# Kernel optimization log

Hardware: AMD Instinct MI355X
Metric: run time of the kernel (lower is better)

Reference implementation:

```python
import jax, jax.numpy as jnp
import numpy as np

EPS = 1e-5

def _patches(x, k, stride, pad):
    # x: [B, C, H, W] -> [B, L, C*k*k] with patch features ordered (c, kh, kw)
    # matching torch unfold / adder2d weight layout [Cout, Cin, kh, kw].
    B, C, H, W = x.shape
    xp = jnp.pad(x, ((0, 0), (0, 0), (pad, pad), (pad, pad)))
    Ho = (H + 2 * pad - k) // stride + 1
    Wo = (W + 2 * pad - k) // stride + 1
    cols = [xp[:, :, i:i + stride * Ho:stride, j:j + stride * Wo:stride]
            for i in range(k) for j in range(k)]
    p = jnp.stack(cols, axis=2)                      # [B, C, k*k, Ho, Wo]
    p = p.reshape(B, C * k * k, Ho * Wo)             # [B, K, L]
    return p.transpose(0, 2, 1), Ho, Wo              # [B, L, K]


def adder2d(x, w, stride, pad):
    # AdderNet layer: out[n,co,h,w] = -sum_{ci,kh,kw} |x_patch - w[co]|
    B = x.shape[0]
    Cout, Cin, k, _ = w.shape
    P, Ho, Wo = _patches(x, k, stride, pad)          # [B, L, K]
    Wf = w.reshape(Cout, Cin * k * k)                # [Cout, K]

    @jax.checkpoint
    def per_out(wrow):                               # wrow: [K]
        return -jnp.sum(jnp.abs(P - wrow), axis=-1)  # [B, L]

    out = jax.lax.map(per_out, Wf)                   # [Cout, B, L]
    return out.transpose(1, 0, 2).reshape(B, Cout, Ho, Wo)


def batchnorm(x, gamma, beta):
    # training-mode BatchNorm2d: batch statistics over (N, H, W)
    mu = jnp.mean(x, axis=(0, 2, 3), keepdims=True)
    var = jnp.var(x, axis=(0, 2, 3), keepdims=True)
    xn = (x - mu) * jax.lax.rsqrt(var + EPS)
    return xn * gamma[None, :, None, None] + beta[None, :, None, None]


def setup_inputs() -> dict:
    key = jax.random.key(0)
    kx, kw1, kw2 = jax.random.split(key, 3)
    B, C, H, W = 32, 64, 32, 32
    return {
        "x": jax.random.normal(kx, (B, C, H, W), dtype=jnp.float32),
        "w1": jax.random.normal(kw1, (C, C, 3, 3), dtype=jnp.float32),
        "g1": jnp.ones((C,), dtype=jnp.float32),
        "b1": jnp.zeros((C,), dtype=jnp.float32),
        "w2": jax.random.normal(kw2, (C, C, 3, 3), dtype=jnp.float32),
        "g2": jnp.ones((C,), dtype=jnp.float32),
        "b2": jnp.zeros((C,), dtype=jnp.float32),
    }


def reference(x, w1, g1, b1, w2, g2, b2):
    out = adder2d(x, w1, stride=1, pad=1)
    out = jax.nn.relu(batchnorm(out, g1, b1))
    out = adder2d(out, w2, stride=1, pad=1)
    out = batchnorm(out, g2, b2)
    return jax.nn.relu(out + x)
```

## Files before the change

kernel.cpp:

```cpp
#include <hip/hip_runtime.h>

#define CH    64
#define HWHW  1024
#define CHW   65536
#define NPIX  32768.0f
#define KDIM  576

#define QSCALE 524288.0f
#define QBIAS  4194304.5f
#define Q0     4194304u
#define QINV   1.9073486328125e-6f

__device__ __forceinline__ unsigned quantf(float x) {
  return (unsigned)fmaf(x, QSCALE, QBIAS);
}

__device__ __forceinline__ unsigned sad_acc(unsigned x, unsigned w, unsigned a) {
  unsigned d;
  asm("v_sad_u32 %0, %1, %2, %3" : "=v"(d) : "v"(x), "s"(w), "v"(a));
  return d;
}

__global__ __launch_bounds__(256) void prep_kernel(
    const float* __restrict__ w1, const float* __restrict__ w2,
    unsigned* __restrict__ wt1, unsigned* __restrict__ wt2,
    float* __restrict__ stats) {
  int i = blockIdx.x * 256 + threadIdx.x;
  if (i < 256) stats[i] = 0.0f;
  if (i < CH * KDIM) {
    int co = i / KDIM, k = i % KDIM;
    wt1[k * CH + co] = quantf(w1[i]);
    wt2[k * CH + co] = quantf(w2[i]);
  }
}

__global__ __launch_bounds__(256, 4) void adder_kernel(
    const float* __restrict__ xin,
    const unsigned* __restrict__ wt,
    float* __restrict__ out,
    float* __restrict__ stats) {
  const int cog  = blockIdx.x;
  const int rg   = blockIdx.y;
  const int n    = blockIdx.z;
  const int tid  = threadIdx.x;
  const int lane = tid & 63;
  const int wv   = __builtin_amdgcn_readfirstlane(tid >> 6);
  const int co0  = cog * 4;
  const int r0   = lane >> 3;
  const int c0   = (lane & 7) * 4;

  __shared__ unsigned xs[2][4][10][37];
  __shared__ unsigned red[64][17];
  const int XSHALF = 4 * 10 * 37;

  const int i0 = tid,       ws0 = i0 / 80, rem0 = i0 % 80;
  const int row0 = rem0 >> 3, c40 = rem0 & 7;
  const int hr0 = rg * 8 - 1 + row0;
  const int i1 = tid + 256, ws1 = i1 / 80, rem1 = i1 % 80;
  const int row1 = rem1 >> 3, c41 = rem1 & 7;
  const int hr1 = rg * 8 - 1 + row1;
  const bool val0 = (hr0 >= 0) && (hr0 < 32);
  const bool val1 = (tid < 64) && (hr1 >= 0) && (hr1 < 32);
  const float* g0 = xin + n * CHW + ws0 * 16 * HWHW + hr0 * 32 + c40 * 4;
  const float* g1 = xin + n * CHW + ws1 * 16 * HWHW + hr1 * 32 + c41 * 4;
  unsigned* l0 = &xs[0][ws0][row0][1 + c40 * 4];
  unsigned* l1 = &xs[0][ws1][row1][1 + c41 * 4];

  float4 a0, a1;
  if (val0) a0 = *(const float4*)g0;
  if (val1) a1 = *(const float4*)g1;
  {
    unsigned* p = (unsigned*)xs;
    for (int i = tid; i < 2 * XSHALF; i += 256) p[i] = Q0;
  }
  __syncthreads();
  if (val0) { l0[0] = quantf(a0.x); l0[1] = quantf(a0.y); l0[2] = quantf(a0.z); l0[3] = quantf(a0.w); }
  if (val1) { l1[0] = quantf(a1.x); l1[1] = quantf(a1.y); l1[2] = quantf(a1.z); l1[3] = quantf(a1.w); }
  __syncthreads();

  const unsigned* wtb = wt + (wv * 144) * 64 + co0;
  unsigned wA[12], wB[12];
  auto LOADW = [&](unsigned* dst, int p) {
    const unsigned* wp = wtb + p * 192;
#pragma unroll
    for (int kw = 0; kw < 3; ++kw)
#pragma unroll
      for (int co = 0; co < 4; ++co) dst[kw * 4 + co] = wp[kw * 64 + co];
  };

  unsigned acc[4][4];
#pragma unroll
  for (int co = 0; co < 4; ++co)
#pragma unroll
    for (int j = 0; j < 4; ++j) acc[co][j] = 0u;

  auto COMPUTE = [&](const unsigned* w, int bufsel, int kh) {
    unsigned xv[6];
#pragma unroll
    for (int j = 0; j < 6; ++j) xv[j] = xs[bufsel][wv][r0 + kh][c0 + j];
#pragma unroll
    for (int kw = 0; kw < 3; ++kw)
#pragma unroll
      for (int co = 0; co < 4; ++co) {
        unsigned ww = w[kw * 4 + co];
        acc[co][0] = sad_acc(xv[kw + 0], ww, acc[co][0]);
        acc[co][1] = sad_acc(xv[kw + 1], ww, acc[co][1]);
        acc[co][2] = sad_acc(xv[kw + 2], ww, acc[co][2]);
        acc[co][3] = sad_acc(xv[kw + 3], ww, acc[co][3]);
      }
  };

  LOADW(wA, 0);
  for (int ci = 0; ci < 16; ci += 2) {
    const int p = ci * 3;
    float4 b0, b1;
    if (val0) b0 = *(const float4*)(g0 + (ci + 1) * HWHW);
    if (val1) b1 = *(const float4*)(g1 + (ci + 1) * HWHW);
    LOADW(wB, p + 1);
    COMPUTE(wA, 0, 0);
    LOADW(wA, p + 2);
    COMPUTE(wB, 0, 1);
    LOADW(wB, p + 3);
    COMPUTE(wA, 0, 2);
    if (val0) { unsigned* d = l0 + XSHALF; d[0] = quantf(b0.x); d[1] = quantf(b0.y); d[2] = quantf(b0.z); d[3] = quantf(b0.w); }
    if (val1) { unsigned* d = l1 + XSHALF; d[0] = quantf(b1.x); d[1] = quantf(b1.y); d[2] = quantf(b1.z); d[3] = quantf(b1.w); }
    __syncthreads();
    const bool more = (ci + 2) < 16;
    float4 e0, e1;
    if (more && val0) e0 = *(const float4*)(g0 + (ci + 2) * HWHW);
    if (more && val1) e1 = *(const float4*)(g1 + (ci + 2) * HWHW);
    LOADW(wA, p + 4);
    COMPUTE(wB, 1, 0);
    LOADW(wB, p + 5);
    COMPUTE(wA, 1, 1);
    { int pn = more ? p + 6 : 0; LOADW(wA, pn); }
    COMPUTE(wB, 1, 2);
    if (more && val0) { l0[0] = quantf(e0.x); l0[1] = quantf(e0.y); l0[2] = quantf(e0.z); l0[3] = quantf(e0.w); }
    if (more && val1) { l1[0] = quantf(e1.x); l1[1] = quantf(e1.y); l1[2] = quantf(e1.z); l1[3] = quantf(e1.w); }
    __syncthreads();
  }

  unsigned* af = &acc[0][0];
  for (int src = 1; src < 4; ++src) {
    if (wv == src) {
#pragma unroll
      for (int j = 0; j < 16; ++j) red[lane][j] = af[j];
    }
    __syncthreads();
    if (wv == 0) {
#pragma unroll
      for (int j = 0; j < 16; ++j) af[j] += red[lane][j];
    }
    __syncthreads();
  }

  if (wv == 0) {
    const int ob = n * CHW + (rg * 8 + r0) * 32 + c0;
#pragma unroll
    for (int co = 0; co < 4; ++co) {
      float t0 = -(float)acc[co][0] * QINV;
      float t1 = -(float)acc[co][1] * QINV;
      float t2 = -(float)acc[co][2] * QINV;
      float t3 = -(float)acc[co][3] * QINV;
      *(float4*)(out + ob + (co0 + co) * HWHW) = make_float4(t0, t1, t2, t3);
      float sm = t0 + t1 + t2 + t3;
      float sq = t0 * t0 + t1 * t1 + t2 * t2 + t3 * t3;
#pragma unroll
      for (int m = 1; m < 64; m <<= 1) {
        sm += __shfl_xor(sm, m);
        sq += __shfl_xor(sq, m);
      }
      if (lane == 0) {
        atomicAdd(stats + co0 + co, sm);
        atomicAdd(stats + 64 + co0 + co, sq);
      }
    }
  }
}

__global__ __launch_bounds__(256) void bnrelu_kernel(
    const float* __restrict__ A, const float* __restrict__ stats,
    const float* __restrict__ g, const float* __restrict__ b,
    float* __restrict__ B) {
  int i = blockIdx.x * 256 + threadIdx.x;
  int c = (i >> 8) & 63;
  float mu  = stats[c] * (1.0f / NPIX);
  float var = fmaf(-mu, mu, stats[64 + c] * (1.0f / NPIX));
  float rs  = rsqrtf(var + 1e-5f);
  float ga  = g[c] * rs;
  float be  = fmaf(-mu, ga, b[c]);
  float4 v = ((const float4*)A)[i];
  v.x = fmaxf(fmaf(v.x, ga, be), 0.0f);
  v.y = fmaxf(fmaf(v.y, ga, be), 0.0f);
  v.z = fmaxf(fmaf(v.z, ga, be), 0.0f);
  v.w = fmaxf(fmaf(v.w, ga, be), 0.0f);
  ((float4*)B)[i] = v;
}

__global__ __launch_bounds__(256) void final_kernel(
    const float* __restrict__ Cbuf, const float* __restrict__ stats,
    const float* __restrict__ g, const float* __restrict__ b,
    const float* __restrict__ xres, float* __restrict__ out) {
  int i = blockIdx.x * 256 + threadIdx.x;
  int c = (i >> 8) & 63;
  float mu  = stats[c] * (1.0f / NPIX);
  float var = fmaf(-mu, mu, stats[64 + c] * (1.0f / NPIX));
  float rs  = rsqrtf(var + 1e-5f);
  float ga  = g[c] * rs;
  float be  = fmaf(-mu, ga, b[c]);
  float4 v = ((const float4*)Cbuf)[i];
  float4 xr = ((const float4*)xres)[i];
  v.x = fmaxf(fmaf(v.x, ga, be) + xr.x, 0.0f);
  v.y = fmaxf(fmaf(v.y, ga, be) + xr.y, 0.0f);
  v.z = fmaxf(fmaf(v.z, ga, be) + xr.z, 0.0f);
  v.w = fmaxf(fmaf(v.w, ga, be) + xr.w, 0.0f);
  ((float4*)out)[i] = v;
}

extern "C" void kernel_launch(void* const* d_in, const int* in_sizes, int n_in,
                              void* d_out, int out_size, void* d_ws, size_t ws_size,
                              hipStream_t stream) {
  const float* x  = (const float*)d_in[0];
  const float* w1 = (const float*)d_in[1];
  const float* g1 = (const float*)d_in[2];
  const float* b1 = (const float*)d_in[3];
  const float* w2 = (const float*)d_in[4];
  const float* g2 = (const float*)d_in[5];
  const float* b2 = (const float*)d_in[6];
  float* outp = (float*)d_out;

  float* ws = (float*)d_ws;
  const size_t NEL = 2097152;
  float*    bufA  = ws;
  float*    bufB  = ws + NEL;
  unsigned* wt1   = (unsigned*)(ws + 2 * NEL);
  unsigned* wt2   = wt1 + CH * KDIM;
  float*    stats = (float*)(wt2 + CH * KDIM);

  prep_kernel<<<144, 256, 0, stream>>>(w1, w2, wt1, wt2, stats);

  dim3 agrid(16, 4, 32);
  adder_kernel<<<agrid, 256, 0, stream>>>(x, wt1, bufA, stats);
  bnrelu_kernel<<<2048, 256, 0, stream>>>(bufA, stats, g1, b1, bufB);
  adder_kernel<<<agrid, 256, 0, stream>>>(bufB, wt2, bufA, stats + 128);
  final_kernel<<<2048, 256, 0, stream>>>(bufA, stats + 128, g2, b2, x, outp);
}
```

Baseline: 171.8 us.

## Stage per-block weights in LDS and vectorize LDS reads for SAD loop

Repacks the quantized weights so each 4-output-channel group is contiguous, copies that group into shared memory once per block, and reads weights with 128-bit LDS loads instead of scalar global loads. The input tile row is padded to 40 entries so activation reads can use uint4/uint2 vector loads. The v_sad operand constraint changes from SGPR to VGPR, since the weights now come from LDS per wave. This adds about 9KB of LDS per block, which may reduce occupancy, and the weights now sit in VGPRs rather than SGPRs.

New measurement: 159.0 us. 7.4% less time.

```diff
diff --git a/kernel.cpp b/kernel.cpp
--- a/kernel.cpp
+++ b/kernel.cpp
@@ -17,7 +17,7 @@
 
 __device__ __forceinline__ unsigned sad_acc(unsigned x, unsigned w, unsigned a) {
   unsigned d;
-  asm("v_sad_u32 %0, %1, %2, %3" : "=v"(d) : "v"(x), "s"(w), "v"(a));
+  asm("v_sad_u32 %0, %1, %2, %3" : "=v"(d) : "v"(x), "v"(w), "v"(a));
   return d;
 }
 
@@ -29,8 +29,9 @@
   if (i < 256) stats[i] = 0.0f;
   if (i < CH * KDIM) {
     int co = i / KDIM, k = i % KDIM;
-    wt1[k * CH + co] = quantf(w1[i]);
-    wt2[k * CH + co] = quantf(w2[i]);
+    int dst = (co >> 2) * 2304 + k * 4 + (co & 3);
+    wt1[dst] = quantf(w1[i]);
+    wt2[dst] = quantf(w2[i]);
   }
 }
 
@@ -49,9 +50,10 @@
   const int r0   = lane >> 3;
   const int c0   = (lane & 7) * 4;
 
-  __shared__ unsigned xs[2][4][10][37];
+  __shared__ unsigned xs[2][4][10][40];
+  __shared__ unsigned wl[2304];
   __shared__ unsigned red[64][17];
-  const int XSHALF = 4 * 10 * 37;
+  const int XSHALF = 4 * 10 * 40;
 
   const int i0 = tid,       ws0 = i0 / 80, rem0 = i0 % 80;
   const int row0 = rem0 >> 3, c40 = rem0 & 7;
@@ -66,6 +68,11 @@
   unsigned* l0 = &xs[0][ws0][row0][1 + c40 * 4];
   unsigned* l1 = &xs[0][ws1][row1][1 + c41 * 4];
 
+  {
+    const uint4* wsrc = (const uint4*)(wt + cog * 2304);
+    uint4* wdst = (uint4*)wl;
+    for (int i = tid; i < 576; i += 256) wdst[i] = wsrc[i];
+  }
   float4 a0, a1;
   if (val0) a0 = *(const float4*)g0;
   if (val1) a1 = *(const float4*)g1;
@@ -78,14 +85,13 @@
   if (val1) { l1[0] = quantf(a1.x); l1[1] = quantf(a1.y); l1[2] = quantf(a1.z); l1[3] = quantf(a1.w); }
   __syncthreads();
 
-  const unsigned* wtb = wt + (wv * 144) * 64 + co0;
   unsigned wA[12], wB[12];
-  auto LOADW = [&](unsigned* dst, int p) {
-    const unsigned* wp = wtb + p * 192;
-#pragma unroll
-    for (int kw = 0; kw < 3; ++kw)
-#pragma unroll
-      for (int co = 0; co < 4; ++co) dst[kw * 4 + co] = wp[kw * 64 + co];
+  auto LOADW = [&](unsigned* dst, int ph) {
+    const uint4* wp = (const uint4*)(wl + ph * 12);
+    uint4 a = wp[0], b = wp[1], c = wp[2];
+    dst[0] = a.x; dst[1] = a.y; dst[2]  = a.z; dst[3]  = a.w;
+    dst[4] = b.x; dst[5] = b.y; dst[6]  = b.z; dst[7]  = b.w;
+    dst[8] = c.x; dst[9] = c.y; dst[10] = c.z; dst[11] = c.w;
   };
 
   unsigned acc[4][4];
@@ -95,9 +101,10 @@
     for (int j = 0; j < 4; ++j) acc[co][j] = 0u;
 
   auto COMPUTE = [&](const unsigned* w, int bufsel, int kh) {
-    unsigned xv[6];
-#pragma unroll
-    for (int j = 0; j < 6; ++j) xv[j] = xs[bufsel][wv][r0 + kh][c0 + j];
+    const unsigned* rowp = &xs[bufsel][wv][r0 + kh][c0];
+    uint4 x4 = *(const uint4*)rowp;
+    uint2 x2 = *(const uint2*)(rowp + 4);
+    unsigned xv[6] = {x4.x, x4.y, x4.z, x4.w, x2.x, x2.y};
 #pragma unroll
     for (int kw = 0; kw < 3; ++kw)
 #pragma unroll
@@ -110,9 +117,10 @@
       }
   };
 
-  LOADW(wA, 0);
+  const int PB = wv * 48;
+  LOADW(wA, PB);
   for (int ci = 0; ci < 16; ci += 2) {
-    const int p = ci * 3;
+    const int p = PB + ci * 3;
     float4 b0, b1;
     if (val0) b0 = *(const float4*)(g0 + (ci + 1) * HWHW);
     if (val1) b1 = *(const float4*)(g1 + (ci + 1) * HWHW);
@@ -133,7 +141,7 @@
     COMPUTE(wB, 1, 0);
     LOADW(wB, p + 5);
     COMPUTE(wA, 1, 1);
-    { int pn = more ? p + 6 : 0; LOADW(wA, pn); }
+    { int pn = more ? p + 6 : PB; LOADW(wA, pn); }
     COMPUTE(wB, 1, 2);
     if (more && val0) { l0[0] = quantf(e0.x); l0[1] = quantf(e0.y); l0[2] = quantf(e0.z); l0[3] = quantf(e0.w); }
     if (more && val1) { l1[0] = quantf(e1.x); l1[1] = quantf(e1.y); l1[2] = quantf(e1.z); l1[3] = quantf(e1.w); }
```
